# Kernel tuning notes

Measured on AMD Instinct MI355X. Metric: run time of the kernel, lower is better.

Reference implementation:

```python
import jax, jax.numpy as jnp
import numpy as np

N_HEAD = 16
ROPE_BASE = 10000.0


def _rope_tables(T, head_dim, dtype):
    inv_freq = 1.0 / (ROPE_BASE ** (jnp.arange(0, head_dim, 2, dtype=jnp.float32) / head_dim))
    t = jnp.arange(T, dtype=jnp.float32)
    freqs = t[:, None] * inv_freq[None, :]          # [T, hd/2]
    emb = jnp.concatenate([freqs, freqs], axis=-1)  # [T, hd]
    return jnp.cos(emb).astype(dtype), jnp.sin(emb).astype(dtype)


def _rotate_half(x):
    h = x.shape[-1] // 2
    return jnp.concatenate([-x[..., h:], x[..., :h]], axis=-1)


def setup_inputs() -> dict:
    key = jax.random.key(0)
    k1, k2, k3 = jax.random.split(key, 3)
    B, T, C = 2, 2048, 1024
    x = jax.random.normal(k1, (B, T, C), dtype=jnp.float32)
    w_attn = jax.random.normal(k2, (3 * C, C), dtype=jnp.float32) * (1.0 / np.sqrt(C))
    w_proj = jax.random.normal(k3, (C, C), dtype=jnp.float32) * (1.0 / np.sqrt(C))
    return {"x": x, "w_attn": w_attn, "w_proj": w_proj}


def reference(x, w_attn, w_proj):
    B, T, C = x.shape
    H = N_HEAD
    hd = C // H

    qkv = jnp.einsum('btc,fc->btf', x, w_attn)          # [B,T,3C]
    q, k, v = jnp.split(qkv, 3, axis=-1)
    # [B,H,T,hd]
    q = q.reshape(B, T, H, hd).transpose(0, 2, 1, 3)
    k = k.reshape(B, T, H, hd).transpose(0, 2, 1, 3)
    v = v.reshape(B, T, H, hd).transpose(0, 2, 1, 3)

    cos, sin = _rope_tables(T, hd, x.dtype)             # [T,hd]
    cos = cos[None, None]
    sin = sin[None, None]
    q = q * cos + _rotate_half(q) * sin
    k = k * cos + _rotate_half(k) * sin

    scale = 1.0 / np.sqrt(hd)
    scores = jnp.einsum('bhqd,bhkd->bhqk', q, k) * scale  # [B,H,T,T]
    causal = jnp.tril(jnp.ones((T, T), dtype=bool))
    scores = jnp.where(causal[None, None], scores, jnp.finfo(scores.dtype).min)
    attn = jax.nn.softmax(scores, axis=-1)
    out = jnp.einsum('bhqk,bhkd->bhqd', attn, v)          # [B,H,T,hd]
    out = out.transpose(0, 2, 1, 3).reshape(B, T, C)
    return jnp.einsum('btc,oc->bto', out, w_proj)
```

## Files before the change

### kernel.cpp

```cpp
#include <hip/hip_runtime.h>
#include <hip/hip_bf16.h>
#include <stdint.h>

typedef unsigned short u16;
typedef __bf16 bf16x8 __attribute__((ext_vector_type(8)));
typedef float f32x4 __attribute__((ext_vector_type(4)));

#define B_ 2
#define T_ 2048
#define C_ 1024
#define H_ 16
#define HD 64
#define M_ (B_ * T_)
#define N3 (3 * C_)

__device__ __forceinline__ float bf2f(u16 u) {
  return __uint_as_float(((unsigned int)u) << 16);
}
__device__ __forceinline__ u16 f2bf(float f) {
  unsigned int u = __float_as_uint(f);
  u += 0x7FFF + ((u >> 16) & 1);
  return (u16)(u >> 16);
}
__device__ __forceinline__ unsigned cvt_pk_bf16(float lo, float hi) {
  unsigned r;
  asm("v_cvt_pk_bf16_f32 %0, %1, %2" : "=v"(r) : "v"(lo), "v"(hi));
  return r;
}
__device__ __forceinline__ void async16(void* ldsp, const void* gp) {
  __builtin_amdgcn_global_load_lds(
      (const __attribute__((address_space(1))) unsigned int*)gp,
      (__attribute__((address_space(3))) unsigned int*)ldsp, 16, 0, 0);
}

union U16x8 { uint4 v; u16 u[8]; };

__device__ __forceinline__ bf16x8 ldsAfrag(const char* base, int row, int kbyte) {
  int off = (row * 128 + kbyte) ^ ((row & 7) << 4);
  uint4 t = *reinterpret_cast<const uint4*>(base + off);
  return __builtin_bit_cast(bf16x8, t);
}
__device__ __forceinline__ bf16x8 ldsRead(const char* p) {
  uint4 t = *reinterpret_cast<const uint4*>(p);
  return __builtin_bit_cast(bf16x8, t);
}

__global__ void cvt_bf16(const float* __restrict__ src, u16* __restrict__ dst, int n4) {
  int i = blockIdx.x * blockDim.x + threadIdx.x;
  int stride = gridDim.x * blockDim.x;
  for (; i < n4; i += stride) {
    float4 v = reinterpret_cast<const float4*>(src)[i];
    uint2 o;
    o.x = (unsigned)f2bf(v.x) | ((unsigned)f2bf(v.y) << 16);
    o.y = (unsigned)f2bf(v.z) | ((unsigned)f2bf(v.w) << 16);
    reinterpret_cast<uint2*>(dst)[i] = o;
  }
}

__global__ void rope_tables_kernel(float* __restrict__ cosT, float* __restrict__ sinT) {
  int t = blockIdx.x;
  int i = threadIdx.x;
  float inv = powf(10000.0f, -(float)i * (1.0f / 32.0f));
  float f = (float)t * inv;
  cosT[t * 32 + i] = cosf(f);
  sinT[t * 32 + i] = sinf(f);
}

template <bool OUT_F32>
__global__ __launch_bounds__(256) void gemm_bt(const u16* __restrict__ A,
                                               const u16* __restrict__ Bw,
                                               void* __restrict__ Cout,
                                               int M, int N, int K) {
  __shared__ uint4 ldsbuf[2048];
  char* As = (char*)ldsbuf;
  char* Bs = (char*)ldsbuf + 16384;
  const int tid = threadIdx.x;
  const int lane = tid & 63;
  const int wv = tid >> 6;
  const int wr = wv >> 1, wc = wv & 1;
  const int lrow = lane & 15, lgrp = lane >> 4;
  const long m0 = (long)blockIdx.x * 128, n0 = (long)blockIdx.y * 128;
  const int srow_l = lane >> 3;
  const int csrc = ((lane & 7) ^ (lane >> 3)) * 8;
  f32x4 acc[4][4] = {};
  for (int k0 = 0; k0 < K; k0 += 64) {
    __syncthreads();
#pragma unroll
    for (int p = 0; p < 4; ++p) {
      int seg = wv * 4 + p;
      int row = seg * 8 + srow_l;
      async16(As + seg * 1024, A + (size_t)(m0 + row) * K + k0 + csrc);
      async16(Bs + seg * 1024, Bw + (size_t)(n0 + row) * K + k0 + csrc);
    }
    __syncthreads();
#pragma unroll
    for (int ks = 0; ks < 2; ++ks) {
      bf16x8 af[4], bfr[4];
#pragma unroll
      for (int i = 0; i < 4; ++i) {
        af[i]  = ldsAfrag(As, wr * 64 + i * 16 + lrow, ks * 64 + lgrp * 16);
        bfr[i] = ldsAfrag(Bs, wc * 64 + i * 16 + lrow, ks * 64 + lgrp * 16);
      }
#pragma unroll
      for (int i = 0; i < 4; ++i)
#pragma unroll
        for (int j = 0; j < 4; ++j)
          acc[i][j] = __builtin_amdgcn_mfma_f32_16x16x32_bf16(af[i], bfr[j], acc[i][j], 0, 0, 0);
    }
  }
#pragma unroll
  for (int i = 0; i < 4; ++i)
#pragma unroll
    for (int j = 0; j < 4; ++j) {
      long r0 = m0 + wr * 64 + i * 16 + lgrp * 4;
      long c  = n0 + wc * 64 + j * 16 + lrow;
#pragma unroll
      for (int r = 0; r < 4; ++r) {
        float v = acc[i][j][r];
        if (OUT_F32)
          ((float*)Cout)[(r0 + r) * N + c] = v;
        else
          ((u16*)Cout)[(r0 + r) * N + c] = f2bf(v);
      }
    }
}

__global__ __launch_bounds__(256) void rope_reshape(const u16* __restrict__ qkv,
                                                    const float* __restrict__ cosT,
                                                    const float* __restrict__ sinT,
                                                    u16* __restrict__ Q,
                                                    u16* __restrict__ K,
                                                    u16* __restrict__ Vt) {
  __shared__ u16 Vs[64][80];
  const float SCLQ = 0.125f * 1.4426950408889634f;
  const int tid = threadIdx.x;
  const int tblk = blockIdx.x, bh = blockIdx.y;
  const int b = bh >> 4, h = bh & 15;
  const int tl = tid >> 2, quar = tid & 3;
  const int t = tblk * 64 + tl;
  const u16* rowp = qkv + ((size_t)(b * T_ + t)) * N3 + h * HD;
  const int d0 = quar * 8;
  float cs[8], sn[8];
#pragma unroll
  for (int j = 0; j < 8; ++j) {
    cs[j] = cosT[t * 32 + d0 + j];
    sn[j] = sinT[t * 32 + d0 + j];
  }
#pragma unroll
  for (int part = 0; part < 2; ++part) {
    const u16* p = rowp + part * C_;
    U16x8 x1, x2, o1, o2;
    x1.v = *reinterpret_cast<const uint4*>(p + d0);
    x2.v = *reinterpret_cast<const uint4*>(p + d0 + 32);
#pragma unroll
    for (int j = 0; j < 8; ++j) {
      float a = bf2f(x1.u[j]), c2 = bf2f(x2.u[j]);
      float f1 = a * cs[j] - c2 * sn[j];
      float f2 = c2 * cs[j] + a * sn[j];
      if (part == 0) { f1 *= SCLQ; f2 *= SCLQ; }
      o1.u[j] = f2bf(f1);
      o2.u[j] = f2bf(f2);
    }
    u16* dst = (part ? K : Q) + ((size_t)bh * T_ + t) * HD;
    *reinterpret_cast<uint4*>(dst + d0) = o1.v;
    *reinterpret_cast<uint4*>(dst + d0 + 32) = o2.v;
  }
  const u16* pv = rowp + 2 * C_;
#pragma unroll
  for (int c = 0; c < 2; ++c) {
    int d = quar * 16 + c * 8;
    *reinterpret_cast<uint4*>(&Vs[tl][d]) = *reinterpret_cast<const uint4*>(pv + d);
  }
  __syncthreads();
  const int d = tid >> 2, tq = tid & 3;
  U16x8 a, bv;
#pragma unroll
  for (int j = 0; j < 8; ++j) a.u[j] = Vs[tq * 16 + j][d];
#pragma unroll
  for (int j = 0; j < 8; ++j) bv.u[j] = Vs[tq * 16 + 8 + j][d];
  u16* dstv = Vt + ((size_t)bh * HD + d) * T_ + tblk * 64 + tq * 16;
  *reinterpret_cast<uint4*>(dstv) = a.v;
  *reinterpret_cast<uint4*>(dstv + 8) = bv.v;
}

__global__ __launch_bounds__(256) void attn_fwd8(const u16* __restrict__ Q,
                                                 const u16* __restrict__ K,
                                                 const u16* __restrict__ Vt,
                                                 u16* __restrict__ O) {
  __shared__ uint4 lds4[5120];
  char* ldsb = (char*)lds4;
  const int tid = threadIdx.x;
  const int lane = tid & 63, wv = tid >> 6;
  const int lrow = lane & 15, lgrp = lane >> 4;
  char* Ps = ldsb + 65536 + wv * 4096;
  const int bh = blockIdx.y;
  const int b = bh >> 4, h = bh & 15;
  const u16* Qh = Q + (size_t)bh * T_ * HD;
  const u16* Kh = K + (size_t)bh * T_ * HD;
  const u16* Vh = Vt + (size_t)bh * HD * T_;

  const int kc_src = ((lane & 7) ^ (lane >> 3)) * 8;
  const int krow_l = lane >> 3;
  const int vrow_l = lane >> 4;

  auto stage = [&](int bufsel, int k0s) {
    char* Kd = ldsb + (bufsel << 15);
    char* Vd = Kd + 16384;
    const u16* Kg = Kh + (size_t)k0s * HD;
    const u16* Vg = Vh + k0s;
#pragma unroll
    for (int seg = 0; seg < 4; ++seg) {
      const u16* gk = Kg + (size_t)(wv * 32 + seg * 8 + krow_l) * HD + kc_src;
      async16(Kd + wv * 4096 + seg * 1024, gk);
      int d = wv * 16 + seg * 4 + vrow_l;
      const u16* gv = Vg + (size_t)d * T_ + ((lane & 15) ^ (d & 7)) * 8;
      async16(Vd + wv * 4096 + seg * 1024, gv);
    }
  };

  const int swz = (lrow & 7) << 4;
  const int kread_a = lrow * 128 + ((lgrp * 16) ^ swz);
  const int kread_b = lrow * 128 + ((64 + lgrp * 16) ^ swz);
  const int vread_a = 16384 + lrow * 256 + ((lgrp * 16) ^ swz);
  const int vread_b = 16384 + lrow * 256 + ((64 + lgrp * 16) ^ swz);
  const char* pa_a = Ps + lrow * 256 + ((lgrp * 16) ^ swz);
  const char* pa_b = Ps + lrow * 256 + ((64 + lgrp * 16) ^ swz);
  char* pw0 = Ps + lrow * 256 + (((0 * 32 + lgrp * 8)) ^ swz);
  char* pw1 = Ps + lrow * 256 + (((1 * 32 + lgrp * 8)) ^ swz);
  char* pw2 = Ps + lrow * 256 + (((2 * 32 + lgrp * 8)) ^ swz);
  char* pw3 = Ps + lrow * 256 + (((3 * 32 + lgrp * 8)) ^ swz);

  uint4 ones4;
  ones4.x = ones4.y = ones4.z = ones4.w = 0x3F803F80u;
  const bf16x8 ones8 = __builtin_bit_cast(bf16x8, ones4);
  int cur = 0;

#pragma unroll
  for (int uu = 0; uu < 2; ++uu) {
    const int unit = uu ? (31 - (int)blockIdx.x) : (int)blockIdx.x;
    const int qs = unit * 64;
    const int q_glob = qs + wv * 16 + lrow;
    bf16x8 qf[2];
#pragma unroll
    for (int ks = 0; ks < 2; ++ks) {
      uint4 t4 = *reinterpret_cast<const uint4*>(
          Qh + (size_t)(qs + wv * 16 + lrow) * HD + ks * 32 + lgrp * 8);
      qf[ks] = __builtin_bit_cast(bf16x8, t4);
    }
    f32x4 o[4] = {};
    f32x4 lacc = {};
    const int niter = (unit >> 1) + 1;

    stage(cur, 0);
    __syncthreads();

    for (int kt = 0; kt < niter; ++kt) {
      const int k0 = kt * 128;
      if (kt + 1 < niter) stage(cur ^ 1, k0 + 128);
      const char* Kb = ldsb + (cur << 15);
      const char* KbA = Kb + kread_a;
      const char* KbB = Kb + kread_b;
      const char* VbA = Kb + vread_a;
      const char* VbB = Kb + vread_b;

      f32x4 s[8] = {};
      __builtin_amdgcn_s_setprio(1);
#pragma unroll
      for (int n = 0; n < 8; ++n)
        s[n] = __builtin_amdgcn_mfma_f32_16x16x32_bf16(ldsRead(KbA + n * 2048), qf[0], s[n], 0, 0, 0);
#pragma unroll
      for (int n = 0; n < 8; ++n)
        s[n] = __builtin_amdgcn_mfma_f32_16x16x32_bf16(ldsRead(KbB + n * 2048), qf[1], s[n], 0, 0, 0);
      __builtin_amdgcn_s_setprio(0);

      const bool diag = (kt == niter - 1);
      if (diag) {
#pragma unroll
        for (int n = 0; n < 8; ++n)
#pragma unroll
          for (int r = 0; r < 4; ++r) {
            int kg = k0 + n * 16 + lgrp * 4 + r;
            float v = (kg <= q_glob) ? s[n][r] : -__builtin_inff();
            s[n][r] = exp2f(v);
          }
      } else {
#pragma unroll
        for (int n = 0; n < 8; ++n)
#pragma unroll
          for (int r = 0; r < 4; ++r) s[n][r] = exp2f(s[n][r]);
      }

#pragma unroll
      for (int n = 0; n < 8; ++n) {
        uint2 w;
        w.x = cvt_pk_bf16(s[n][0], s[n][1]);
        w.y = cvt_pk_bf16(s[n][2], s[n][3]);
        char* pwb = (n & 3) == 0 ? pw0 : (n & 3) == 1 ? pw1 : (n & 3) == 2 ? pw2 : pw3;
        *reinterpret_cast<uint2*>(pwb + (n >> 2) * 128) = w;
      }

      __builtin_amdgcn_s_setprio(1);
#pragma unroll
      for (int ks = 0; ks < 4; ++ks) {
        const char* pab = (ks & 1) ? pa_b : pa_a;
        const char* vbb = (ks & 1) ? VbB : VbA;
        bf16x8 pa = ldsRead(pab + (ks >> 1) * 128);
        lacc = __builtin_amdgcn_mfma_f32_16x16x32_bf16(pa, ones8, lacc, 0, 0, 0);
#pragma unroll
        for (int dn = 0; dn < 4; ++dn) {
          bf16x8 bv = ldsRead(vbb + dn * 4096 + (ks >> 1) * 128);
          o[dn] = __builtin_amdgcn_mfma_f32_16x16x32_bf16(pa, bv, o[dn], 0, 0, 0);
        }
      }
      __builtin_amdgcn_s_setprio(0);
      __syncthreads();
      cur ^= 1;
    }

#pragma unroll
    for (int r = 0; r < 4; ++r) {
      float inv = 1.0f / lacc[r];
      int t = qs + wv * 16 + lgrp * 4 + r;
#pragma unroll
      for (int dn = 0; dn < 4; ++dn) {
        int c = h * HD + dn * 16 + lrow;
        O[((size_t)(b * T_ + t)) * C_ + c] = f2bf(o[dn][r] * inv);
      }
    }
  }
}

extern "C" void kernel_launch(void* const* d_in, const int* in_sizes, int n_in,
                              void* d_out, int out_size, void* d_ws, size_t ws_size,
                              hipStream_t stream) {
  const float* x  = (const float*)d_in[0];
  const float* wa = (const float*)d_in[1];
  const float* wp = (const float*)d_in[2];
  float* out = (float*)d_out;
  char* ws = (char*)d_ws;
  size_t off = 0;
  auto alloc = [&](size_t bytes) {
    char* p = ws + off;
    off += (bytes + 255) & ~(size_t)255;
    return p;
  };
  u16* xb   = (u16*)alloc((size_t)M_ * C_ * 2);
  u16* wab  = (u16*)alloc((size_t)N3 * C_ * 2);
  u16* wpb  = (u16*)alloc((size_t)C_ * C_ * 2);
  u16* qkvb = (u16*)alloc((size_t)M_ * N3 * 2);
  u16* Qb   = (u16*)alloc((size_t)B_ * H_ * T_ * HD * 2);
  u16* Kb   = (u16*)alloc((size_t)B_ * H_ * T_ * HD * 2);
  u16* Vtb  = (u16*)alloc((size_t)B_ * H_ * T_ * HD * 2);
  u16* Ob   = (u16*)alloc((size_t)M_ * C_ * 2);
  float* cosT = (float*)alloc((size_t)T_ * 32 * 4);
  float* sinT = (float*)alloc((size_t)T_ * 32 * 4);
  (void)in_sizes; (void)n_in; (void)out_size; (void)ws_size;

  cvt_bf16<<<1024, 256, 0, stream>>>(x, xb, M_ * C_ / 4);
  cvt_bf16<<<1024, 256, 0, stream>>>(wa, wab, N3 * C_ / 4);
  cvt_bf16<<<512, 256, 0, stream>>>(wp, wpb, C_ * C_ / 4);
  rope_tables_kernel<<<T_, 32, 0, stream>>>(cosT, sinT);
  gemm_bt<false><<<dim3(M_ / 128, N3 / 128), 256, 0, stream>>>(xb, wab, qkvb, M_, N3, C_);
  rope_reshape<<<dim3(T_ / 64, B_ * H_), 256, 0, stream>>>(qkvb, cosT, sinT, Qb, Kb, Vtb);
  attn_fwd8<<<dim3(16, B_ * H_), 256, 0, stream>>>(Qb, Kb, Vtb, Ob);
  gemm_bt<true><<<dim3(M_ / 128, C_ / 128), 256, 0, stream>>>(Ob, wpb, out, M_, C_, C_);
}
```

Before: 128.0 us.

## Use 64-key tiles with 4-slot async prefetch pipeline in attention

The attention kernel's KV tile shrinks from 128 to 64 keys, and loads now go through a four-slot ring buffer that prefetches three tiles ahead instead of double buffering. Explicit vmcnt waits plus a raw s_barrier replace __syncthreads. The aim is to hide global-to-LDS load latency better and to make the causal diagonal tile less wasteful. The cost is twice as many loop iterations and barriers, each doing less MFMA work, and extra pressure on the LDS budget.

```diff
diff --git a/kernel.cpp b/kernel.cpp
--- a/kernel.cpp
+++ b/kernel.cpp
@@ -13,6 +13,8 @@
 #define HD 64
 #define M_ (B_ * T_)
 #define N3 (3 * C_)
+
+#define WAITV(N) asm volatile("s_waitcnt vmcnt(" #N ")" ::: "memory")
 
 __device__ __forceinline__ float bf2f(u16 u) {
   return __uint_as_float(((unsigned int)u) << 16);
@@ -183,63 +185,61 @@
   *reinterpret_cast<uint4*>(dstv + 8) = bv.v;
 }
 
-__global__ __launch_bounds__(256) void attn_fwd8(const u16* __restrict__ Q,
+__global__ __launch_bounds__(256) void attn_fwd9(const u16* __restrict__ Q,
                                                  const u16* __restrict__ K,
                                                  const u16* __restrict__ Vt,
                                                  u16* __restrict__ O) {
-  __shared__ uint4 lds4[5120];
+  __shared__ uint4 lds4[4608];
   char* ldsb = (char*)lds4;
   const int tid = threadIdx.x;
   const int lane = tid & 63, wv = tid >> 6;
   const int lrow = lane & 15, lgrp = lane >> 4;
-  char* Ps = ldsb + 65536 + wv * 4096;
   const int bh = blockIdx.y;
   const int b = bh >> 4, h = bh & 15;
   const u16* Qh = Q + (size_t)bh * T_ * HD;
   const u16* Kh = K + (size_t)bh * T_ * HD;
   const u16* Vh = Vt + (size_t)bh * HD * T_;
 
-  const int kc_src = ((lane & 7) ^ (lane >> 3)) * 8;
-  const int krow_l = lane >> 3;
-  const int vrow_l = lane >> 4;
-
-  auto stage = [&](int bufsel, int k0s) {
-    char* Kd = ldsb + (bufsel << 15);
-    char* Vd = Kd + 16384;
-    const u16* Kg = Kh + (size_t)k0s * HD;
-    const u16* Vg = Vh + k0s;
-#pragma unroll
-    for (int seg = 0; seg < 4; ++seg) {
-      const u16* gk = Kg + (size_t)(wv * 32 + seg * 8 + krow_l) * HD + kc_src;
-      async16(Kd + wv * 4096 + seg * 1024, gk);
-      int d = wv * 16 + seg * 4 + vrow_l;
-      const u16* gv = Vg + (size_t)d * T_ + ((lane & 15) ^ (d & 7)) * 8;
-      async16(Vd + wv * 4096 + seg * 1024, gv);
+  const int srow_l = lane >> 3;
+  const int csrc = ((lane & 7) ^ (lane >> 3)) * 8;
+
+  auto stage = [&](int slot, int kt) {
+    char* Kd = ldsb + (slot << 14);
+    char* Vd = Kd + 8192;
+    const u16* Kg = Kh + (size_t)(kt * 64) * HD;
+    const u16* Vg = Vh + kt * 64;
+#pragma unroll
+    for (int seg = 0; seg < 2; ++seg) {
+      int row = wv * 16 + seg * 8 + srow_l;
+      async16(Kd + wv * 2048 + seg * 1024, Kg + (size_t)row * HD + csrc);
+      async16(Vd + wv * 2048 + seg * 1024, Vg + (size_t)row * T_ + csrc);
     }
   };
 
   const int swz = (lrow & 7) << 4;
-  const int kread_a = lrow * 128 + ((lgrp * 16) ^ swz);
-  const int kread_b = lrow * 128 + ((64 + lgrp * 16) ^ swz);
-  const int vread_a = 16384 + lrow * 256 + ((lgrp * 16) ^ swz);
-  const int vread_b = 16384 + lrow * 256 + ((64 + lgrp * 16) ^ swz);
-  const char* pa_a = Ps + lrow * 256 + ((lgrp * 16) ^ swz);
-  const char* pa_b = Ps + lrow * 256 + ((64 + lgrp * 16) ^ swz);
-  char* pw0 = Ps + lrow * 256 + (((0 * 32 + lgrp * 8)) ^ swz);
-  char* pw1 = Ps + lrow * 256 + (((1 * 32 + lgrp * 8)) ^ swz);
-  char* pw2 = Ps + lrow * 256 + (((2 * 32 + lgrp * 8)) ^ swz);
-  char* pw3 = Ps + lrow * 256 + (((3 * 32 + lgrp * 8)) ^ swz);
+  const int krA = lrow * 128 + ((lgrp * 16) ^ swz);
+  const int krB = lrow * 128 + ((64 + lgrp * 16) ^ swz);
+  const int vrA = 8192 + krA;
+  const int vrB = 8192 + krB;
+  char* PsW = ldsb + 65536 + wv * 2048 + lrow * 128;
+  char* pw0 = PsW + ((0 * 32 + lgrp * 8) ^ swz);
+  char* pw1 = PsW + ((1 * 32 + lgrp * 8) ^ swz);
+  char* pw2 = PsW + ((2 * 32 + lgrp * 8) ^ swz);
+  char* pw3 = PsW + ((3 * 32 + lgrp * 8) ^ swz);
+  const char* paA = PsW + ((lgrp * 16) ^ swz);
+  const char* paB = PsW + ((64 + lgrp * 16) ^ swz);
 
   uint4 ones4;
   ones4.x = ones4.y = ones4.z = ones4.w = 0x3F803F80u;
   const bf16x8 ones8 = __builtin_bit_cast(bf16x8, ones4);
-  int cur = 0;
 
 #pragma unroll
   for (int uu = 0; uu < 2; ++uu) {
     const int unit = uu ? (31 - (int)blockIdx.x) : (int)blockIdx.x;
     const int qs = unit * 64;
     const int q_glob = qs + wv * 16 + lrow;
+    const int nu = unit + 1;
+
     bf16x8 qf[2];
 #pragma unroll
     for (int ks = 0; ks < 2; ++ks) {
@@ -249,72 +249,80 @@
     }
     f32x4 o[4] = {};
     f32x4 lacc = {};
-    const int niter = (unit >> 1) + 1;
-
-    stage(cur, 0);
-    __syncthreads();
-
-    for (int kt = 0; kt < niter; ++kt) {
-      const int k0 = kt * 128;
-      if (kt + 1 < niter) stage(cur ^ 1, k0 + 128);
-      const char* Kb = ldsb + (cur << 15);
-      const char* KbA = Kb + kread_a;
-      const char* KbB = Kb + kread_b;
-      const char* VbA = Kb + vread_a;
-      const char* VbB = Kb + vread_b;
-
-      f32x4 s[8] = {};
+
+    {
+      const int pre = nu < 3 ? nu : 3;
+      for (int i = 0; i < pre; ++i) stage(i, i);
+      WAITV(0);
+      __builtin_amdgcn_s_barrier();
+      __builtin_amdgcn_sched_barrier(0);
+    }
+
+    for (int kt = 0; kt < nu; ++kt) {
+      if (kt + 3 < nu) stage((kt + 3) & 3, kt + 3);
+      const char* buf = ldsb + ((kt & 3) << 14);
+      const char* KbA = buf + krA;
+      const char* KbB = buf + krB;
+      const char* VbA = buf + vrA;
+      const char* VbB = buf + vrB;
+
+      f32x4 s[4] = {};
       __builtin_amdgcn_s_setprio(1);
 #pragma unroll
-      for (int n = 0; n < 8; ++n)
+      for (int n = 0; n < 4; ++n)
         s[n] = __builtin_amdgcn_mfma_f32_16x16x32_bf16(ldsRead(KbA + n * 2048), qf[0], s[n], 0, 0, 0);
 #pragma unroll
-      for (int n = 0; n < 8; ++n)
+      for (int n = 0; n < 4; ++n)
         s[n] = __builtin_amdgcn_mfma_f32_16x16x32_bf16(ldsRead(KbB + n * 2048), qf[1], s[n], 0, 0, 0);
       __builtin_amdgcn_s_setprio(0);
 
-      const bool diag = (kt == niter - 1);
-      if (diag) {
-#pragma unroll
-        for (int n = 0; n < 8; ++n)
+      if (kt == nu - 1) {
+#pragma unroll
+        for (int n = 0; n < 4; ++n)
 #pragma unroll
           for (int r = 0; r < 4; ++r) {
-            int kg = k0 + n * 16 + lgrp * 4 + r;
+            int kg = kt * 64 + n * 16 + lgrp * 4 + r;
             float v = (kg <= q_glob) ? s[n][r] : -__builtin_inff();
             s[n][r] = exp2f(v);
           }
       } else {
 #pragma unroll
-        for (int n = 0; n < 8; ++n)
+        for (int n = 0; n < 4; ++n)
 #pragma unroll
           for (int r = 0; r < 4; ++r) s[n][r] = exp2f(s[n][r]);
       }
 
-#pragma unroll
-      for (int n = 0; n < 8; ++n) {
-        uint2 w;
-        w.x = cvt_pk_bf16(s[n][0], s[n][1]);
-        w.y = cvt_pk_bf16(s[n][2], s[n][3]);
-        char* pwb = (n & 3) == 0 ? pw0 : (n & 3) == 1 ? pw1 : (n & 3) == 2 ? pw2 : pw3;
-        *reinterpret_cast<uint2*>(pwb + (n >> 2) * 128) = w;
+      {
+        uint2 w0, w1, w2, w3;
+        w0.x = cvt_pk_bf16(s[0][0], s[0][1]); w0.y = cvt_pk_bf16(s[0][2], s[0][3]);
+        w1.x = cvt_pk_bf16(s[1][0], s[1][1]); w1.y = cvt_pk_bf16(s[1][2], s[1][3]);
+        w2.x = cvt_pk_bf16(s[2][0], s[2][1]); w2.y = cvt_pk_bf16(s[2][2], s[2][3]);
+        w3.x = cvt_pk_bf16(s[3][0], s[3][1]); w3.y = cvt_pk_bf16(s[3][2], s[3][3]);
+        *reinterpret_cast<uint2*>(pw0) = w0;
+        *reinterpret_cast<uint2*>(pw1) = w1;
+        *reinterpret_cast<uint2*>(pw2) = w2;
+        *reinterpret_cast<uint2*>(pw3) = w3;
       }
 
       __builtin_amdgcn_s_setprio(1);
 #pragma unroll
-      for (int ks = 0; ks < 4; ++ks) {
-        const char* pab = (ks & 1) ? pa_b : pa_a;
-        const char* vbb = (ks & 1) ? VbB : VbA;
-        bf16x8 pa = ldsRead(pab + (ks >> 1) * 128);
+      for (int ks = 0; ks < 2; ++ks) {
+        bf16x8 pa = ldsRead(ks ? paB : paA);
         lacc = __builtin_amdgcn_mfma_f32_16x16x32_bf16(pa, ones8, lacc, 0, 0, 0);
+        const char* vbb = ks ? VbB : VbA;
 #pragma unroll
         for (int dn = 0; dn < 4; ++dn) {
-          bf16x8 bv = ldsRead(vbb + dn * 4096 + (ks >> 1) * 128);
+          bf16x8 bv = ldsRead(vbb + dn * 2048);
           o[dn] = __builtin_amdgcn_mfma_f32_16x16x32_bf16(pa, bv, o[dn], 0, 0, 0);
         }
       }
       __builtin_amdgcn_s_setprio(0);
-      __syncthreads();
-      cur ^= 1;
+
+      if (kt + 4 <= nu)      WAITV(8);
+      else if (kt + 3 == nu) WAITV(4);
+      else                   WAITV(0);
+      __builtin_amdgcn_s_barrier();
+      __builtin_amdgcn_sched_barrier(0);
     }
 
 #pragma unroll
@@ -362,6 +370,6 @@
   rope_tables_kernel<<<T_, 32, 0, stream>>>(cosT, sinT);
   gemm_bt<false><<<dim3(M_ / 128, N3 / 128), 256, 0, stream>>>(xb, wab, qkvb, M_, N3, C_);
   rope_reshape<<<dim3(T_ / 64, B_ * H_), 256, 0, stream>>>(qkvb, cosT, sinT, Qb, Kb, Vtb);
-  attn_fwd8<<<dim3(16, B_ * H_), 256, 0, stream>>>(Qb, Kb, Vtb, Ob);
+  attn_fwd9<<<dim3(16, B_ * H_), 256, 0, stream>>>(Qb, Kb, Vtb, Ob);
   gemm_bt<true><<<dim3(M_ / 128, C_ / 128), 256, 0, stream>>>(Ob, wpb, out, M_, C_, C_);
 }
```

After: 128.7 us. No clear change (+0.5%).
